# Performance work log

Hardware: AMD Instinct MI355X
Metric: run time of the kernel (lower is better)

Reference implementation:

```python
import jax, jax.numpy as jnp
import numpy as np

N = 100000
E = 1600000
F_IN = 128
NHID = 50
NOUT = 50


def gcn_conv(x, W, b, src, dst, n):
    # x: [N, Fin] -> transform first (PyG GCNConv order)
    h = x @ W  # [N, Fout]
    # symmetric normalization with self-loops already included in src/dst
    ones = jnp.ones(src.shape[0], dtype=h.dtype)
    deg = jax.ops.segment_sum(ones, dst, num_segments=n)  # in-degree incl self-loop
    dinv = jnp.where(deg > 0, jax.lax.rsqrt(deg), 0.0)
    norm = dinv[src] * dinv[dst]  # [E']
    msgs = h[src] * norm[:, None]  # gather + scale, [E', Fout]
    out = jax.ops.segment_sum(msgs, dst, num_segments=n)  # scatter-add
    return out + b


def setup_inputs() -> dict:
    key = jax.random.key(0)
    k1, k2, k3, k4, k5, k6 = jax.random.split(key, 6)
    x = jax.random.normal(k1, (N, F_IN), dtype=jnp.float32)
    edge_index = jax.random.randint(k2, (2, E), 0, N, dtype=jnp.int64) if jax.config.read('jax_enable_x64') else jax.random.randint(k2, (2, E), 0, N, dtype=jnp.int32)
    # Glorot-ish init for weights
    W1 = jax.random.normal(k3, (F_IN, NHID), dtype=jnp.float32) * (1.0 / np.sqrt(F_IN))
    b1 = jnp.zeros((NHID,), dtype=jnp.float32)
    W2 = jax.random.normal(k4, (NHID, NOUT), dtype=jnp.float32) * (1.0 / np.sqrt(NHID))
    b2 = jnp.zeros((NOUT,), dtype=jnp.float32)
    return {"x": x, "W1": W1, "b1": b1, "W2": W2, "b2": b2, "edge_index": edge_index}


def reference(x, W1, b1, W2, b2, edge_index):
    n = x.shape[0]
    # add self-loops once (shared by both layers)
    loop = jnp.arange(n, dtype=edge_index.dtype)
    src = jnp.concatenate([edge_index[0], loop])
    dst = jnp.concatenate([edge_index[1], loop])
    h = gcn_conv(x, W1, b1, src, dst, n)
    h = jax.nn.relu(h)
    # dropout is identity in eval mode (training=False)
    out = gcn_conv(h, W2, b2, src, dst, n)
    return out
```

## Files before the change

### kernel.cpp

```cpp
#include <hip/hip_runtime.h>
#include <hip/hip_fp16.h>

#define FIN 128
#define FH 50
#define HSTRIDE 64
#define MAXNB 1024
#define BSHIFT 7
#define BSIZE 128
#define CAP 3072
#define PCHUNK 4096
#define SRCMASK 0x01FFFFFFu


__global__ __launch_bounds__(256) void partition_kernel(const int* __restrict__ src,
                                                        const int* __restrict__ dst,
                                                        int* __restrict__ gcursor,
                                                        unsigned int* __restrict__ packed,
                                                        int E, int NB) {
    __shared__ int hist[MAXNB];
    __shared__ int wbase[MAXNB];
    int t = threadIdx.x;
    int base = blockIdx.x * PCHUNK;
    for (int i = t; i < NB; i += 256) hist[i] = 0;
    __syncthreads();
#pragma unroll 4
    for (int i = 0; i < PCHUNK / 256; i++) {
        int e = base + t + i * 256;
        if (e < E) atomicAdd(&hist[dst[e] >> BSHIFT], 1);
    }
    __syncthreads();
    for (int i = t; i < NB; i += 256) {
        int c = hist[i];
        wbase[i] = c ? atomicAdd(&gcursor[i], c) : 0;
        hist[i] = 0;
    }
    __syncthreads();
#pragma unroll 4
    for (int i = 0; i < PCHUNK / 256; i++) {
        int e = base + t + i * 256;
        if (e < E) {
            unsigned int s = (unsigned int)src[e];
            int d = dst[e];
            int b = d >> BSHIFT;
            int off = atomicAdd(&hist[b], 1);
            packed[(size_t)b * CAP + wbase[b] + off] =
                ((unsigned int)(d & (BSIZE - 1)) << 25) | s;
        }
    }
}

__global__ __launch_bounds__(256) void bucket_build_kernel(const unsigned int* __restrict__ packed,
                                                           const int* __restrict__ gcursor,
                                                           int* __restrict__ rbeg,
                                                           int* __restrict__ rend,
                                                           float* __restrict__ dinv,
                                                           int* __restrict__ csr, int n) {
    __shared__ int degl[BSIZE];
    __shared__ int excl[BSIZE];
    __shared__ int lcur[BSIZE];
    int b = blockIdx.x;
    int t = threadIdx.x;
    int nbeg = b << BSHIFT;
    int sbase = b * CAP;
    int cnt = gcursor[b];
    if (t < BSIZE) degl[t] = 0;
    __syncthreads();
    for (int e = t; e < cnt; e += 256)
        atomicAdd(&degl[packed[sbase + e] >> 25], 1);
    __syncthreads();
    int v = (t < BSIZE) ? degl[t] : 0;
    if (t < BSIZE) excl[t] = v;
    __syncthreads();
    for (int off = 1; off < BSIZE; off <<= 1) {
        int add = (t >= off && t < BSIZE) ? excl[t - off] : 0;
        __syncthreads();
        if (t < BSIZE) excl[t] += add;
        __syncthreads();
    }
    if (t < BSIZE) {
        int ex = excl[t] - v;
        int node = nbeg + t;
        if (node < n) {
            rbeg[node] = sbase + ex;
            rend[node] = sbase + ex + v;
            dinv[node] = rsqrtf((float)v + 1.0f);
        }
        lcur[t] = ex;
    }
    __syncthreads();
    for (int e = t; e < cnt; e += 256) {
        unsigned int w = packed[sbase + e];
        int off = atomicAdd(&lcur[w >> 25], 1);
        csr[sbase + off] = (int)(w & SRCMASK);
    }
}


__global__ __launch_bounds__(256) void gemm1_kernel(
    const float* __restrict__ x, const float* __restrict__ W,
    const float* __restrict__ dinv, __half* __restrict__ hs1,
    __half* __restrict__ hs2, int n) {
    int t = threadIdx.x;
    if (blockIdx.x == 0) {
        if (t < HSTRIDE)           hs1[((size_t)n << 6) + t] = __float2half(0.f);
        else if (t < 2 * HSTRIDE)  hs2[((size_t)n << 6) + (t - HSTRIDE)] = __float2half(0.f);
    }
    int row = blockIdx.x * 256 + t;
    if (row >= n) return;
    float a[FH];
#pragma unroll
    for (int c = 0; c < FH; c++) a[c] = 0.f;
    const float4* xr = (const float4*)(x + (size_t)row * FIN);
    for (int k4 = 0; k4 < FIN / 4; k4++) {
        float4 xv = xr[k4];
        float xs[4] = {xv.x, xv.y, xv.z, xv.w};
#pragma unroll
        for (int kk = 0; kk < 4; kk++) {
            const float* w0 = W + (k4 * 4 + kk) * FH;
#pragma unroll
            for (int c = 0; c < FH; c++)
                a[c] = fmaf(xs[kk], w0[c], a[c]);
        }
    }
    float dv = dinv[row];
    __half2* hp = (__half2*)(hs1 + ((size_t)row << 6));
#pragma unroll
    for (int c = 0; c < HSTRIDE / 2; c++) {
        float lo = (2 * c     < FH) ? a[2 * c] * dv     : 0.f;
        float hi = (2 * c + 1 < FH) ? a[2 * c + 1] * dv : 0.f;
        hp[c] = __floats2half2_rn(lo, hi);
    }
}

__global__ __launch_bounds__(256) void gemm2_kernel(
    const float* __restrict__ h1, const float* __restrict__ W,
    const float* __restrict__ dinv, __half* __restrict__ hs2, int n) {
    int t = threadIdx.x;
    int row = blockIdx.x * 256 + t;
    if (row >= n) return;
    const float2* xp = (const float2*)(h1 + (size_t)row * FH);
    float xr[FH];
#pragma unroll
    for (int k2 = 0; k2 < FH / 2; k2++) {
        float2 v = xp[k2];
        xr[2 * k2]     = v.x;
        xr[2 * k2 + 1] = v.y;
    }
    float a[FH];
#pragma unroll
    for (int c = 0; c < FH; c++) a[c] = 0.f;
    for (int k = 0; k < FH; k++) {
        const float* w0 = W + k * FH;
        float xs = xr[k];
#pragma unroll
        for (int c = 0; c < FH; c++)
            a[c] = fmaf(xs, w0[c], a[c]);
    }
    float dv = dinv[row];
    __half2* hp = (__half2*)(hs2 + ((size_t)row << 6));
#pragma unroll
    for (int c = 0; c < FH / 2; c++)
        hp[c] = __floats2half2_rn(a[2 * c] * dv, a[2 * c + 1] * dv);
}

__global__ __launch_bounds__(256) void gather_kernel(
    const __half* __restrict__ hs, const int* __restrict__ rbeg,
    const int* __restrict__ rend, const int* __restrict__ csr,
    const float* __restrict__ dinv, const float* __restrict__ b,
    float* __restrict__ out, int n, int do_relu) {
    int wid = blockIdx.x * 4 + (threadIdx.x >> 6);
    int lane = threadIdx.x & 63;
    if (wid >= n) return;
    int beg = rbeg[wid];
    int end = rend[wid];
    float acc = __half2float(hs[((size_t)wid << 6) + lane]);
    for (int base = beg; base < end; base += 64) {
        int rem = end - base;
        int idx = (lane < rem) ? csr[base + lane] : n;
        int cnt = rem < 64 ? rem : 64;
        for (int j = 0; j < cnt; j += 16) {
            float v[16];
#pragma unroll
            for (int u = 0; u < 16; u++) {
                int s = __shfl(idx, j + u);
                v[u] = __half2float(hs[((size_t)s << 6) + lane]);
            }
            float s01 = (v[0] + v[1]) + (v[2] + v[3]);
            float s23 = (v[4] + v[5]) + (v[6] + v[7]);
            float s45 = (v[8] + v[9]) + (v[10] + v[11]);
            float s67 = (v[12] + v[13]) + (v[14] + v[15]);
            acc += (s01 + s23) + (s45 + s67);
        }
    }
    if (lane < FH) {
        float o = fmaf(dinv[wid], acc, b[lane]);
        if (do_relu) o = fmaxf(o, 0.f);
        out[(size_t)wid * FH + lane] = o;
    }
}

extern "C" void kernel_launch(void* const* d_in, const int* in_sizes, int n_in,
                              void* d_out, int out_size, void* d_ws, size_t ws_size,
                              hipStream_t stream) {
    const float* x  = (const float*)d_in[0];
    const float* W1 = (const float*)d_in[1];
    const float* b1 = (const float*)d_in[2];
    const float* W2 = (const float*)d_in[3];
    const float* b2 = (const float*)d_in[4];
    const int*   ei = (const int*)d_in[5];

    int n = in_sizes[0] / FIN;
    int E = in_sizes[5] / 2;
    const int* src = ei;
    const int* dst = ei + E;
    int NB = (n + BSIZE - 1) >> BSHIFT;

    char* ws = (char*)d_ws;
    size_t off = 0;
    auto alloc = [&](size_t bytes) {
        void* p = ws + off;
        off = (off + bytes + 511) & ~(size_t)511;
        return p;
    };
    size_t hs_bytes   = (size_t)(n + 1) * HSTRIDE * 2;
    size_t slab_bytes = (size_t)NB * CAP * 4;
    size_t un_bytes   = slab_bytes > hs_bytes ? slab_bytes : hs_bytes;

    int*          gcursor = (int*)alloc((size_t)MAXNB * 4);
    int*          rbeg    = (int*)alloc((size_t)n * 4);
    int*          rend    = (int*)alloc((size_t)n * 4);
    float*        dinv    = (float*)alloc((size_t)n * 4);
    int*          csr     = (int*)alloc(slab_bytes);
    __half*       hs1     = (__half*)alloc(hs_bytes);
    void*         un      = alloc(un_bytes);
    unsigned int* packed  = (unsigned int*)un;
    __half*       hs2     = (__half*)un;
    float*        out     = (float*)d_out;

    hipMemsetAsync(gcursor, 0, (size_t)MAXNB * 4, stream);

    int pChunks = (E + PCHUNK - 1) / PCHUNK;
    partition_kernel<<<pChunks, 256, 0, stream>>>(src, dst, gcursor, packed, E, NB);
    bucket_build_kernel<<<NB, 256, 0, stream>>>(packed, gcursor, rbeg, rend, dinv, csr, n);

    int g1Blocks = (n + 255) / 256;
    int g2Blocks = (n + 255) / 256;
    int gatherBlocks = (n + 3) / 4;

    gemm1_kernel<<<g1Blocks, 256, 0, stream>>>(x, W1, dinv, hs1, hs2, n);
    gather_kernel<<<gatherBlocks, 256, 0, stream>>>(hs1, rbeg, rend, csr, dinv, b1, out, n, 1);
    gemm2_kernel<<<g2Blocks, 256, 0, stream>>>(out, W2, dinv, hs2, n);
    gather_kernel<<<gatherBlocks, 256, 0, stream>>>(hs2, rbeg, rend, csr, dinv, b2, out, n, 0);
}
```

Measured before the change: 290.9 us.

## Use transposed fp16 weights and column-pair loop order in dense GEMMs

Adds a small kernel that converts W1 and W2 to transposed half-precision copies. The per-row GEMM kernels now keep the whole input row in registers and loop over output column pairs, reading the weights as half2 pairs. This replaces the 50-wide accumulator array and halves weight load bytes, aiming to cut scalar weight loads and register pressure. It adds one extra launch and rounds the weights to fp16, which loses precision. The 128-float row array may also spill registers.

```diff
diff --git a/kernel.cpp b/kernel.cpp
--- a/kernel.cpp
+++ b/kernel.cpp
@@ -96,8 +96,23 @@
 }
 
 
+__global__ __launch_bounds__(256) void wcvt_kernel(const float* __restrict__ W1,
+                                                   const float* __restrict__ W2,
+                                                   __half* __restrict__ WT1,
+                                                   __half* __restrict__ WT2) {
+    int t = blockIdx.x * 256 + threadIdx.x;
+    if (t < FIN * FH) {
+        int k = t / FH, c = t - k * FH;
+        WT1[c * FIN + k] = __float2half(W1[t]);
+    }
+    if (t < FH * FH) {
+        int k = t / FH, c = t - k * FH;
+        WT2[c * FH + k] = __float2half(W2[t]);
+    }
+}
+
 __global__ __launch_bounds__(256) void gemm1_kernel(
-    const float* __restrict__ x, const float* __restrict__ W,
+    const float* __restrict__ x, const __half* __restrict__ WT,
     const float* __restrict__ dinv, __half* __restrict__ hs1,
     __half* __restrict__ hs2, int n) {
     int t = threadIdx.x;
@@ -107,60 +122,67 @@
     }
     int row = blockIdx.x * 256 + t;
     if (row >= n) return;
-    float a[FH];
-#pragma unroll
-    for (int c = 0; c < FH; c++) a[c] = 0.f;
-    const float4* xr = (const float4*)(x + (size_t)row * FIN);
-    for (int k4 = 0; k4 < FIN / 4; k4++) {
-        float4 xv = xr[k4];
-        float xs[4] = {xv.x, xv.y, xv.z, xv.w};
-#pragma unroll
-        for (int kk = 0; kk < 4; kk++) {
-            const float* w0 = W + (k4 * 4 + kk) * FH;
-#pragma unroll
-            for (int c = 0; c < FH; c++)
-                a[c] = fmaf(xs[kk], w0[c], a[c]);
-        }
+    float xr[FIN];
+    const float4* xp = (const float4*)(x + (size_t)row * FIN);
+#pragma unroll
+    for (int i = 0; i < FIN / 4; i++) {
+        float4 v = xp[i];
+        xr[4 * i]     = v.x;
+        xr[4 * i + 1] = v.y;
+        xr[4 * i + 2] = v.z;
+        xr[4 * i + 3] = v.w;
     }
     float dv = dinv[row];
     __half2* hp = (__half2*)(hs1 + ((size_t)row << 6));
-#pragma unroll
-    for (int c = 0; c < HSTRIDE / 2; c++) {
-        float lo = (2 * c     < FH) ? a[2 * c] * dv     : 0.f;
-        float hi = (2 * c + 1 < FH) ? a[2 * c + 1] * dv : 0.f;
-        hp[c] = __floats2half2_rn(lo, hi);
-    }
+    for (int cp = 0; cp < FH / 2; cp++) {
+        const __half2* w0 = (const __half2*)(WT + (2 * cp) * FIN);
+        const __half2* w1 = (const __half2*)(WT + (2 * cp + 1) * FIN);
+        float a0e = 0.f, a0o = 0.f, a1e = 0.f, a1o = 0.f;
+#pragma unroll
+        for (int k2 = 0; k2 < FIN / 2; k2++) {
+            __half2 p0 = w0[k2], p1 = w1[k2];
+            a0e = fmaf(xr[2 * k2],     __low2float(p0),  a0e);
+            a0o = fmaf(xr[2 * k2 + 1], __high2float(p0), a0o);
+            a1e = fmaf(xr[2 * k2],     __low2float(p1),  a1e);
+            a1o = fmaf(xr[2 * k2 + 1], __high2float(p1), a1o);
+        }
+        hp[cp] = __floats2half2_rn((a0e + a0o) * dv, (a1e + a1o) * dv);
+    }
+#pragma unroll
+    for (int c = FH / 2; c < HSTRIDE / 2; c++)
+        hp[c] = __floats2half2_rn(0.f, 0.f);
 }
 
 __global__ __launch_bounds__(256) void gemm2_kernel(
-    const float* __restrict__ h1, const float* __restrict__ W,
+    const float* __restrict__ h1, const __half* __restrict__ WT,
     const float* __restrict__ dinv, __half* __restrict__ hs2, int n) {
     int t = threadIdx.x;
     int row = blockIdx.x * 256 + t;
     if (row >= n) return;
+    float xr[FH];
     const float2* xp = (const float2*)(h1 + (size_t)row * FH);
-    float xr[FH];
 #pragma unroll
     for (int k2 = 0; k2 < FH / 2; k2++) {
         float2 v = xp[k2];
         xr[2 * k2]     = v.x;
         xr[2 * k2 + 1] = v.y;
     }
-    float a[FH];
-#pragma unroll
-    for (int c = 0; c < FH; c++) a[c] = 0.f;
-    for (int k = 0; k < FH; k++) {
-        const float* w0 = W + k * FH;
-        float xs = xr[k];
-#pragma unroll
-        for (int c = 0; c < FH; c++)
-            a[c] = fmaf(xs, w0[c], a[c]);
-    }
     float dv = dinv[row];
     __half2* hp = (__half2*)(hs2 + ((size_t)row << 6));
-#pragma unroll
-    for (int c = 0; c < FH / 2; c++)
-        hp[c] = __floats2half2_rn(a[2 * c] * dv, a[2 * c + 1] * dv);
+    for (int cp = 0; cp < FH / 2; cp++) {
+        const __half2* w0 = (const __half2*)(WT + (2 * cp) * FH);
+        const __half2* w1 = (const __half2*)(WT + (2 * cp + 1) * FH);
+        float a0e = 0.f, a0o = 0.f, a1e = 0.f, a1o = 0.f;
+#pragma unroll
+        for (int k2 = 0; k2 < FH / 2; k2++) {
+            __half2 p0 = w0[k2], p1 = w1[k2];
+            a0e = fmaf(xr[2 * k2],     __low2float(p0),  a0e);
+            a0o = fmaf(xr[2 * k2 + 1], __high2float(p0), a0o);
+            a1e = fmaf(xr[2 * k2],     __low2float(p1),  a1e);
+            a1o = fmaf(xr[2 * k2 + 1], __high2float(p1), a1o);
+        }
+        hp[cp] = __floats2half2_rn((a0e + a0o) * dv, (a1e + a1o) * dv);
+    }
 }
 
 __global__ __launch_bounds__(256) void gather_kernel(
@@ -232,6 +254,8 @@
     float*        dinv    = (float*)alloc((size_t)n * 4);
     int*          csr     = (int*)alloc(slab_bytes);
     __half*       hs1     = (__half*)alloc(hs_bytes);
+    __half*       wt1     = (__half*)alloc((size_t)FIN * FH * 2);
+    __half*       wt2     = (__half*)alloc((size_t)FH * FH * 2);
     void*         un      = alloc(un_bytes);
     unsigned int* packed  = (unsigned int*)un;
     __half*       hs2     = (__half*)un;
@@ -239,6 +263,8 @@
 
     hipMemsetAsync(gcursor, 0, (size_t)MAXNB * 4, stream);
 
+    wcvt_kernel<<<(FIN * FH + 255) / 256, 256, 0, stream>>>(W1, W2, wt1, wt2);
+
     int pChunks = (E + PCHUNK - 1) / PCHUNK;
     partition_kernel<<<pChunks, 256, 0, stream>>>(src, dst, gcursor, packed, E, NB);
     bucket_build_kernel<<<NB, 256, 0, stream>>>(packed, gcursor, rbeg, rend, dinv, csr, n);
@@ -247,8 +273,8 @@
     int g2Blocks = (n + 255) / 256;
     int gatherBlocks = (n + 3) / 4;
 
-    gemm1_kernel<<<g1Blocks, 256, 0, stream>>>(x, W1, dinv, hs1, hs2, n);
+    gemm1_kernel<<<g1Blocks, 256, 0, stream>>>(x, wt1, dinv, hs1, hs2, n);
     gather_kernel<<<gatherBlocks, 256, 0, stream>>>(hs1, rbeg, rend, csr, dinv, b1, out, n, 1);
-    gemm2_kernel<<<g2Blocks, 256, 0, stream>>>(out, W2, dinv, hs2, n);
+    gemm2_kernel<<<g2Blocks, 256, 0, stream>>>(out, wt2, dinv, hs2, n);
     gather_kernel<<<gatherBlocks, 256, 0, stream>>>(hs2, rbeg, rend, csr, dinv, b2, out, n, 0);
 }
```

Measured after the change: 324.2 us. 11.4% more time.

## Use fp16 MFMA with hi/lo split for both dense GEMMs

Applied to the files above, without the earlier changes.

Replaces the scalar per-row FMA GEMMs with wavefront-level 16x16x32 fp16 MFMA tiles. Each fp32 activation is split into a high and a low fp16 part to keep accuracy close to fp32, while the weights are converted once into fp16 fragment layout by a small new kernel. This moves the dense transform from scalar FMA onto the matrix cores and lowers per-thread register pressure. The cost is an extra launch, fp16 rounding of the weights, and output stores that write scattered half values instead of packed half2 rows.

```diff
diff --git a/kernel.cpp b/kernel.cpp
--- a/kernel.cpp
+++ b/kernel.cpp
@@ -10,6 +10,9 @@
 #define CAP 3072
 #define PCHUNK 4096
 #define SRCMASK 0x01FFFFFFu
+
+typedef _Float16 f16x8 __attribute__((ext_vector_type(8)));
+typedef float f32x4 __attribute__((ext_vector_type(4)));
 
 
 __global__ __launch_bounds__(256) void partition_kernel(const int* __restrict__ src,
@@ -96,8 +99,29 @@
 }
 
 
+__global__ __launch_bounds__(256) void wcvt_kernel(const float* __restrict__ W1,
+                                                   const float* __restrict__ W2,
+                                                   _Float16* __restrict__ WF1,
+                                                   _Float16* __restrict__ WF2) {
+    int idx = blockIdx.x * 256 + threadIdx.x;
+    if (idx < 4 * 4 * 64 * 8) {
+        int i = idx & 7, lane = (idx >> 3) & 63, tile = idx >> 9;
+        int ct = tile & 3, kt = tile >> 2;
+        int k = kt * 32 + ((lane >> 4) << 3) + i;
+        int c = ct * 16 + (lane & 15);
+        WF1[idx] = (c < FH) ? (_Float16)W1[k * FH + c] : (_Float16)0.f;
+    } else if (idx < 8192 + 2 * 4 * 64 * 8) {
+        int g = idx - 8192;
+        int i = g & 7, lane = (g >> 3) & 63, tile = g >> 9;
+        int ct = tile & 3, kt = tile >> 2;
+        int k = kt * 32 + ((lane >> 4) << 3) + i;
+        int c = ct * 16 + (lane & 15);
+        WF2[g] = (k < FH && c < FH) ? (_Float16)W2[k * FH + c] : (_Float16)0.f;
+    }
+}
+
 __global__ __launch_bounds__(256) void gemm1_kernel(
-    const float* __restrict__ x, const float* __restrict__ W,
+    const float* __restrict__ x, const _Float16* __restrict__ WF,
     const float* __restrict__ dinv, __half* __restrict__ hs1,
     __half* __restrict__ hs2, int n) {
     int t = threadIdx.x;
@@ -105,62 +129,123 @@
         if (t < HSTRIDE)           hs1[((size_t)n << 6) + t] = __float2half(0.f);
         else if (t < 2 * HSTRIDE)  hs2[((size_t)n << 6) + (t - HSTRIDE)] = __float2half(0.f);
     }
-    int row = blockIdx.x * 256 + t;
-    if (row >= n) return;
-    float a[FH];
-#pragma unroll
-    for (int c = 0; c < FH; c++) a[c] = 0.f;
-    const float4* xr = (const float4*)(x + (size_t)row * FIN);
-    for (int k4 = 0; k4 < FIN / 4; k4++) {
-        float4 xv = xr[k4];
-        float xs[4] = {xv.x, xv.y, xv.z, xv.w};
-#pragma unroll
-        for (int kk = 0; kk < 4; kk++) {
-            const float* w0 = W + (k4 * 4 + kk) * FH;
-#pragma unroll
-            for (int c = 0; c < FH; c++)
-                a[c] = fmaf(xs[kk], w0[c], a[c]);
-        }
-    }
-    float dv = dinv[row];
-    __half2* hp = (__half2*)(hs1 + ((size_t)row << 6));
-#pragma unroll
-    for (int c = 0; c < HSTRIDE / 2; c++) {
-        float lo = (2 * c     < FH) ? a[2 * c] * dv     : 0.f;
-        float hi = (2 * c + 1 < FH) ? a[2 * c + 1] * dv : 0.f;
-        hp[c] = __floats2half2_rn(lo, hi);
+    int tile = blockIdx.x * 4 + (t >> 6);
+    int l = t & 63;
+    int mt = (n + 15) >> 4;
+    if (tile >= mt) return;
+    int arow = tile * 16 + (l & 15);
+    if (arow >= n) arow = n - 1;
+    const f16x8* WB = (const f16x8*)WF;
+    f32x4 acc[4] = {{0.f,0.f,0.f,0.f},{0.f,0.f,0.f,0.f},
+                    {0.f,0.f,0.f,0.f},{0.f,0.f,0.f,0.f}};
+#pragma unroll
+    for (int kt = 0; kt < 4; kt++) {
+        const float* xp = x + (size_t)arow * FIN + kt * 32 + ((l >> 4) << 3);
+        float4 v0 = *(const float4*)xp;
+        float4 v1 = *(const float4*)(xp + 4);
+        float vs[8] = {v0.x, v0.y, v0.z, v0.w, v1.x, v1.y, v1.z, v1.w};
+        f16x8 hi, lo;
+#pragma unroll
+        for (int i = 0; i < 8; i++) {
+            _Float16 h = (_Float16)vs[i];
+            hi[i] = h;
+            lo[i] = (_Float16)(vs[i] - (float)h);
+        }
+#pragma unroll
+        for (int ct = 0; ct < 4; ct++) {
+            f16x8 b = WB[(kt * 4 + ct) * 64 + l];
+            acc[ct] = __builtin_amdgcn_mfma_f32_16x16x32_f16(hi, b, acc[ct], 0, 0, 0);
+            acc[ct] = __builtin_amdgcn_mfma_f32_16x16x32_f16(lo, b, acc[ct], 0, 0, 0);
+        }
+    }
+    int rbase = tile * 16 + ((l >> 4) << 2);
+    float dv[4];
+#pragma unroll
+    for (int j = 0; j < 4; j++) {
+        int r = rbase + j;
+        dv[j] = dinv[r < n ? r : 0];
+    }
+#pragma unroll
+    for (int ct = 0; ct < 4; ct++) {
+        int col = ct * 16 + (l & 15);
+        if (col < FH) {
+#pragma unroll
+            for (int j = 0; j < 4; j++) {
+                int r = rbase + j;
+                if (r < n)
+                    hs1[((size_t)r << 6) + col] = __float2half(acc[ct][j] * dv[j]);
+            }
+        }
     }
 }
 
 __global__ __launch_bounds__(256) void gemm2_kernel(
-    const float* __restrict__ h1, const float* __restrict__ W,
+    const float* __restrict__ h1, const _Float16* __restrict__ WF,
     const float* __restrict__ dinv, __half* __restrict__ hs2, int n) {
     int t = threadIdx.x;
-    int row = blockIdx.x * 256 + t;
-    if (row >= n) return;
-    const float2* xp = (const float2*)(h1 + (size_t)row * FH);
-    float xr[FH];
-#pragma unroll
-    for (int k2 = 0; k2 < FH / 2; k2++) {
-        float2 v = xp[k2];
-        xr[2 * k2]     = v.x;
-        xr[2 * k2 + 1] = v.y;
-    }
-    float a[FH];
-#pragma unroll
-    for (int c = 0; c < FH; c++) a[c] = 0.f;
-    for (int k = 0; k < FH; k++) {
-        const float* w0 = W + k * FH;
-        float xs = xr[k];
-#pragma unroll
-        for (int c = 0; c < FH; c++)
-            a[c] = fmaf(xs, w0[c], a[c]);
-    }
-    float dv = dinv[row];
-    __half2* hp = (__half2*)(hs2 + ((size_t)row << 6));
-#pragma unroll
-    for (int c = 0; c < FH / 2; c++)
-        hp[c] = __floats2half2_rn(a[2 * c] * dv, a[2 * c + 1] * dv);
+    int tile = blockIdx.x * 4 + (t >> 6);
+    int l = t & 63;
+    int mt = (n + 15) >> 4;
+    if (tile >= mt) return;
+    int arow = tile * 16 + (l & 15);
+    if (arow >= n) arow = n - 1;
+    const f16x8* WB = (const f16x8*)WF;
+    const float* hp = h1 + (size_t)arow * FH;
+    f32x4 acc[4] = {{0.f,0.f,0.f,0.f},{0.f,0.f,0.f,0.f},
+                    {0.f,0.f,0.f,0.f},{0.f,0.f,0.f,0.f}};
+#pragma unroll
+    for (int kt = 0; kt < 2; kt++) {
+        int k0 = kt * 32 + ((l >> 4) << 3);
+        float vs[8];
+        if (kt == 0) {
+            const float2* p2 = (const float2*)(hp + k0);
+#pragma unroll
+            for (int q = 0; q < 4; q++) {
+                float2 v = p2[q];
+                vs[2 * q] = v.x;
+                vs[2 * q + 1] = v.y;
+            }
+        } else {
+#pragma unroll
+            for (int i = 0; i < 8; i++) {
+                int k = k0 + i;
+                float v = hp[k < FH ? k : 0];
+                vs[i] = (k < FH) ? v : 0.f;
+            }
+        }
+        f16x8 hi, lo;
+#pragma unroll
+        for (int i = 0; i < 8; i++) {
+            _Float16 h = (_Float16)vs[i];
+            hi[i] = h;
+            lo[i] = (_Float16)(vs[i] - (float)h);
+        }
+#pragma unroll
+        for (int ct = 0; ct < 4; ct++) {
+            f16x8 b = WB[(kt * 4 + ct) * 64 + l];
+            acc[ct] = __builtin_amdgcn_mfma_f32_16x16x32_f16(hi, b, acc[ct], 0, 0, 0);
+            acc[ct] = __builtin_amdgcn_mfma_f32_16x16x32_f16(lo, b, acc[ct], 0, 0, 0);
+        }
+    }
+    int rbase = tile * 16 + ((l >> 4) << 2);
+    float dv[4];
+#pragma unroll
+    for (int j = 0; j < 4; j++) {
+        int r = rbase + j;
+        dv[j] = dinv[r < n ? r : 0];
+    }
+#pragma unroll
+    for (int ct = 0; ct < 4; ct++) {
+        int col = ct * 16 + (l & 15);
+        if (col < FH) {
+#pragma unroll
+            for (int j = 0; j < 4; j++) {
+                int r = rbase + j;
+                if (r < n)
+                    hs2[((size_t)r << 6) + col] = __float2half(acc[ct][j] * dv[j]);
+            }
+        }
+    }
 }
 
 __global__ __launch_bounds__(256) void gather_kernel(
@@ -232,6 +317,8 @@
     float*        dinv    = (float*)alloc((size_t)n * 4);
     int*          csr     = (int*)alloc(slab_bytes);
     __half*       hs1     = (__half*)alloc(hs_bytes);
+    _Float16*     wf1     = (_Float16*)alloc((size_t)8192 * 2);
+    _Float16*     wf2     = (_Float16*)alloc((size_t)4096 * 2);
     void*         un      = alloc(un_bytes);
     unsigned int* packed  = (unsigned int*)un;
     __half*       hs2     = (__half*)un;
@@ -239,16 +326,18 @@
 
     hipMemsetAsync(gcursor, 0, (size_t)MAXNB * 4, stream);
 
+    wcvt_kernel<<<(8192 + 4096 + 255) / 256, 256, 0, stream>>>(W1, W2, wf1, wf2);
+
     int pChunks = (E + PCHUNK - 1) / PCHUNK;
     partition_kernel<<<pChunks, 256, 0, stream>>>(src, dst, gcursor, packed, E, NB);
     bucket_build_kernel<<<NB, 256, 0, stream>>>(packed, gcursor, rbeg, rend, dinv, csr, n);
 
-    int g1Blocks = (n + 255) / 256;
-    int g2Blocks = (n + 255) / 256;
+    int mt = (n + 15) / 16;
+    int gBlocks = (mt + 3) / 4;
     int gatherBlocks = (n + 3) / 4;
 
-    gemm1_kernel<<<g1Blocks, 256, 0, stream>>>(x, W1, dinv, hs1, hs2, n);
+    gemm1_kernel<<<gBlocks, 256, 0, stream>>>(x, wf1, dinv, hs1, hs2, n);
     gather_kernel<<<gatherBlocks, 256, 0, stream>>>(hs1, rbeg, rend, csr, dinv, b1, out, n, 1);
-    gemm2_kernel<<<g2Blocks, 256, 0, stream>>>(out, W2, dinv, hs2, n);
+    gemm2_kernel<<<gBlocks, 256, 0, stream>>>(out, wf2, dinv, hs2, n);
     gather_kernel<<<gatherBlocks, 256, 0, stream>>>(hs2, rbeg, rend, csr, dinv, b2, out, n, 0);
 }
```

After: 246.5 us. 1.18x faster.
